# Kernel tuning notes

Measured on AMD Instinct MI355X. Metric: run time of the kernel, lower is better.

## Reference

```python
import jax, jax.numpy as jnp
import numpy as np

B, T, H = 1024, 1024, 64


def _lstm_cell(x, h, c, w_ih, w_hh, b_ih, b_hh):
    # gates: [B, 4H] in PyTorch order i, f, g, o
    g = x @ w_ih.T + h @ w_hh.T + b_ih + b_hh
    i, f, gg, o = jnp.split(g, 4, axis=-1)
    i = jax.nn.sigmoid(i)
    f = jax.nn.sigmoid(f)
    gg = jnp.tanh(gg)
    o = jax.nn.sigmoid(o)
    c_new = f * c + i * gg
    h_new = o * jnp.tanh(c_new)
    return h_new, c_new


def setup_inputs() -> dict:
    key = jax.random.key(0)
    ks = jax.random.split(key, 12)
    s = 1.0 / np.sqrt(H)  # torch default init scale
    r = lambda k, shape: jax.random.normal(k, shape, dtype=jnp.float32) * s
    return {
        "x": jax.random.normal(ks[0], (B, T), dtype=jnp.float32),
        "w_ih1": r(ks[1], (4 * H, 1)),
        "w_hh1": r(ks[2], (4 * H, H)),
        "b_ih1": r(ks[3], (4 * H,)),
        "b_hh1": r(ks[4], (4 * H,)),
        "w_ih2": r(ks[5], (4 * H, H)),
        "w_hh2": r(ks[6], (4 * H, H)),
        "b_ih2": r(ks[7], (4 * H,)),
        "b_hh2": r(ks[8], (4 * H,)),
        "w_lin": r(ks[9], (1, H)),
        "b_lin": r(ks[10], (1,)),
        "future_preds": 0,
    }


def reference(x, w_ih1, w_hh1, b_ih1, b_hh1, w_ih2, w_hh2, b_ih2, b_hh2,
              w_lin, b_lin, future_preds):
    bsz = x.shape[0]
    h1 = jnp.zeros((bsz, H), x.dtype)
    c1 = jnp.zeros((bsz, H), x.dtype)
    h2 = jnp.zeros((bsz, H), x.dtype)
    c2 = jnp.zeros((bsz, H), x.dtype)

    def step(carry, x_t):
        h1, c1, h2, c2 = carry
        h1, c1 = _lstm_cell(x_t, h1, c1, w_ih1, w_hh1, b_ih1, b_hh1)
        h2, c2 = _lstm_cell(h1, h2, c2, w_ih2, w_hh2, b_ih2, b_hh2)
        out = h2 @ w_lin.T + b_lin  # [B, 1]
        return (h1, c1, h2, c2), out

    xs = x.T[:, :, None]  # [T, B, 1]
    carry, outs = jax.lax.scan(step, (h1, c1, h2, c2), xs)
    outputs = outs[:, :, 0].T  # [B, T]

    if future_preds > 0:
        last = outs[-1]  # [B, 1]

        def fstep(carry, _):
            h1, c1, h2, c2, prev = carry
            h1, c1 = _lstm_cell(prev, h1, c1, w_ih1, w_hh1, b_ih1, b_hh1)
            h2, c2 = _lstm_cell(h1, h2, c2, w_ih2, w_hh2, b_ih2, b_hh2)
            out = h2 @ w_lin.T + b_lin
            return (h1, c1, h2, c2, out), out

        _, fouts = jax.lax.scan(fstep, (*carry, last), None, length=future_preds)
        outputs = jnp.concatenate([outputs, fouts[:, :, 0].T], axis=1)

    return outputs
```

## Files before the change

kernel.cpp:

```cpp
#include <hip/hip_runtime.h>
#include <hip/hip_bf16.h>


typedef _Float16 f16x8 __attribute__((ext_vector_type(8)));
typedef float    f32x4 __attribute__((ext_vector_type(4)));

namespace {
constexpr int Bb = 1024;
constexpr int Tt = 1024;
constexpr int NBat = 4;
constexpr int HSTR = 72;
constexpr int XSTR = 1025;

__device__ __forceinline__ int srow(int row) {
    return row ^ ((row >> 3) & 7);
}
__device__ __forceinline__ float sigm(float x) {
    float e = __builtin_amdgcn_exp2f(-1.4426950408889634f * x);
    return __builtin_amdgcn_rcpf(1.0f + e);
}
__device__ __forceinline__ float tanh_f(float x) {
    float e = __builtin_amdgcn_exp2f(-2.8853900817779268f * x);
    return __builtin_amdgcn_rcpf(1.0f + e) * 2.0f - 1.0f;
}
__device__ __forceinline__ bool detect_f32(const void* w) {
    const unsigned short* p = (const unsigned short*)w;
    int sane = 0;
    for (int i = 0; i < 64; ++i) {
        int e = (p[2 * i] >> 7) & 0xFF;
        if (e >= 107 && e <= 129) ++sane;
    }
    return sane < 32;
}
__device__ __forceinline__ float ld(const void* p, int i, bool f32) {
    return f32 ? ((const float*)p)[i]
               : __bfloat162float(((const __hip_bfloat16*)p)[i]);
}
__device__ __forceinline__ void st(void* p, int i, float v, bool f32) {
    if (f32) ((float*)p)[i] = v;
    else     ((__hip_bfloat16*)p)[i] = __float2bfloat16(v);
}
}

__global__ __launch_bounds__(512, 1) void lstm2_kernel(
    const void* __restrict__ x,
    const void* __restrict__ w_ih1,
    const void* __restrict__ w_hh1,
    const void* __restrict__ b_ih1,
    const void* __restrict__ b_hh1,
    const void* __restrict__ w_ih2,
    const void* __restrict__ w_hh2,
    const void* __restrict__ b_ih2,
    const void* __restrict__ b_hh2,
    const void* __restrict__ w_lin,
    const void* __restrict__ b_lin,
    void* __restrict__ out)
{
    const int tid  = threadIdx.x;
    const int lane = tid & 63;
    const int w    = tid >> 6;
    const int gw   = w & 3;
    const bool isP = w < 4;
    const int m    = lane & 15;
    const int quad = lane >> 4;
    const int bb   = blockIdx.x * NBat;

    const bool f32 = detect_f32(w_hh1);

    __shared__ float                  xs[NBat * XSTR];
    __shared__ __align__(16) _Float16 h1buf[2][16 * HSTR];
    __shared__ __align__(16) _Float16 h2buf[2][16 * HSTR];
    __shared__ __align__(16) float    scr1[4][64 * 4];
    __shared__ __align__(16) float    scr2[4][64 * 4];
    __shared__ float                  headl[2][16];
    __shared__ float                  outbuf[NBat * Tt];

    for (int i = tid; i < NBat * 1024; i += 512)
        xs[(i >> 10) * XSTR + (i & 1023)] = ld(x, (bb + (i >> 10)) * Tt + (i & 1023), f32);
    for (int i = tid; i < 16 * HSTR; i += 512) {
        h1buf[0][i] = (_Float16)0; h1buf[1][i] = (_Float16)0;
        h2buf[0][i] = (_Float16)0; h2buf[1][i] = (_Float16)0;
    }

    const int arow = lane & 15;
    const int g_ld = arow & 3;
    const int u_ld = arow >> 2;
    f16x8 wfA[4][2], wfB[4][2];
    {
        const void* MA = isP ? w_hh1 : w_ih2;
#pragma unroll
        for (int q = 0; q < 4; ++q) {
            const int row = 64 * g_ld + 16 * gw + 4 * q + u_ld;
#pragma unroll
            for (int s = 0; s < 2; ++s) {
                const int base = row * 64 + 32 * s + quad * 8;
                if (f32) {
                    const float* A = (const float*)MA;
                    const float* B = (const float*)w_hh2;
#pragma unroll
                    for (int j = 0; j < 8; ++j) {
                        wfA[q][s][j] = (_Float16)A[base + j];
                        wfB[q][s][j] = isP ? (_Float16)0.0f : (_Float16)B[base + j];
                    }
                } else {
                    const __hip_bfloat16* A = (const __hip_bfloat16*)MA;
                    const __hip_bfloat16* B = (const __hip_bfloat16*)w_hh2;
#pragma unroll
                    for (int j = 0; j < 8; ++j) {
                        wfA[q][s][j] = (_Float16)__bfloat162float(A[base + j]);
                        wfB[q][s][j] = isP ? (_Float16)0.0f
                                           : (_Float16)__bfloat162float(B[base + j]);
                    }
                }
            }
        }
    }
    f32x4 bv[4], wxv[4];
#pragma unroll
    for (int q = 0; q < 4; ++q)
#pragma unroll
        for (int r = 0; r < 4; ++r) {
            const int row = 64 * r + 16 * gw + 4 * q + quad;
            bv[q][r] = isP ? (ld(b_ih1, row, f32) + ld(b_hh1, row, f32))
                           : (ld(b_ih2, row, f32) + ld(b_hh2, row, f32));
            wxv[q][r] = isP ? ld(w_ih1, row, f32) : 0.0f;
        }
    const int cb = lane >> 4;
    const int uo = lane & 15;
    const int cidx = srow(lane) * 4;
    const float wl_u = ld(w_lin, 16 * gw + uo, f32);
    const float blin = ld(b_lin, 0, f32);
    float cst = 0.0f;
    __syncthreads();

    for (int t = 0; t <= Tt; ++t) {
        if (isP) {
            if (t < Tt) {
                f32x4 acc[4];
                const float xt = xs[(m & (NBat - 1)) * XSTR + t];
#pragma unroll
                for (int q = 0; q < 4; ++q)
#pragma unroll
                    for (int r = 0; r < 4; ++r)
                        acc[q][r] = fmaf(xt, wxv[q][r], bv[q][r]);
                if (t > 0) {
                    const _Float16* hp = h1buf[(t - 1) & 1] + m * HSTR;
                    const f16x8 ba = *(const f16x8*)(hp + quad * 8);
                    const f16x8 bb2 = *(const f16x8*)(hp + 32 + quad * 8);
#pragma unroll
                    for (int q = 0; q < 4; ++q) {
                        acc[q] = __builtin_amdgcn_mfma_f32_16x16x32_f16(wfA[q][0], ba, acc[q], 0, 0, 0);
                        acc[q] = __builtin_amdgcn_mfma_f32_16x16x32_f16(wfA[q][1], bb2, acc[q], 0, 0, 0);
                    }
                }
                if (m < NBat)
#pragma unroll
                    for (int q = 0; q < 4; ++q)
                        *(f32x4*)&scr1[gw][srow(m * 16 + q * 4 + quad) * 4] = acc[q];
                const f32x4 g = *(const f32x4*)&scr1[gw][cidx];
                float ig = sigm(g[0]), fg = sigm(g[1]);
                float gg = tanh_f(g[2]), og = sigm(g[3]);
                cst = fmaf(fg, cst, ig * gg);
                h1buf[t & 1][cb * HSTR + 16 * gw + uo] = (_Float16)(og * tanh_f(cst));
            }
        } else {
            if (t > 0) {
                if (t > 1 && w == 4 && lane < NBat) {
                    float s = blin;
#pragma unroll
                    for (int k = 0; k < 4; ++k) s += headl[t & 1][k * 4 + lane];
                    outbuf[lane * Tt + (t - 2)] = s;
                }
                const _Float16* h1p = h1buf[(t - 1) & 1] + m * HSTR;
                const _Float16* h2p = h2buf[t & 1] + m * HSTR;
                const f16x8 b1a = *(const f16x8*)(h1p + quad * 8);
                const f16x8 b1b = *(const f16x8*)(h1p + 32 + quad * 8);
                const f16x8 b2a = *(const f16x8*)(h2p + quad * 8);
                const f16x8 b2b = *(const f16x8*)(h2p + 32 + quad * 8);
                f32x4 acc[4];
#pragma unroll
                for (int q = 0; q < 4; ++q) {
                    f32x4 p2 = __builtin_amdgcn_mfma_f32_16x16x32_f16(wfA[q][0], b1a, bv[q], 0, 0, 0);
                    p2 = __builtin_amdgcn_mfma_f32_16x16x32_f16(wfA[q][1], b1b, p2, 0, 0, 0);
                    f32x4 p3 = __builtin_amdgcn_mfma_f32_16x16x32_f16(wfB[q][0], b2a, f32x4{0,0,0,0}, 0, 0, 0);
                    p3 = __builtin_amdgcn_mfma_f32_16x16x32_f16(wfB[q][1], b2b, p3, 0, 0, 0);
                    acc[q] = p2 + p3;
                }
                if (m < NBat)
#pragma unroll
                    for (int q = 0; q < 4; ++q)
                        *(f32x4*)&scr2[gw][srow(m * 16 + q * 4 + quad) * 4] = acc[q];
                const f32x4 g = *(const f32x4*)&scr2[gw][cidx];
                float ig = sigm(g[0]), fg = sigm(g[1]);
                float gg = tanh_f(g[2]), og = sigm(g[3]);
                cst = fmaf(fg, cst, ig * gg);
                float h = og * tanh_f(cst);
                h2buf[(t - 1) & 1][cb * HSTR + 16 * gw + uo] = (_Float16)h;
                float p = h * wl_u;
                p += __shfl_xor(p, 1); p += __shfl_xor(p, 2);
                p += __shfl_xor(p, 4); p += __shfl_xor(p, 8);
                if (uo == 0) headl[(t - 1) & 1][gw * 4 + cb] = p;
            }
        }
        __syncthreads();
    }

    if (w == 4 && lane < NBat) {
        float s = blin;
#pragma unroll
        for (int k = 0; k < 4; ++k) s += headl[(Tt - 1) & 1][k * 4 + lane];
        outbuf[lane * Tt + (Tt - 1)] = s;
    }
    __syncthreads();
    for (int i = tid; i < NBat * Tt; i += 512)
        st(out, (bb + (i >> 10)) * Tt + (i & 1023), outbuf[i], f32);
}

extern "C" void kernel_launch(void* const* d_in, const int* in_sizes, int n_in,
                              void* d_out, int out_size, void* d_ws, size_t ws_size,
                              hipStream_t stream)
{
    (void)in_sizes; (void)n_in; (void)out_size; (void)d_ws; (void)ws_size;
    lstm2_kernel<<<dim3(Bb / NBat), dim3(512), 0, stream>>>(
        d_in[0], d_in[1], d_in[2], d_in[3], d_in[4], d_in[5],
        d_in[6], d_in[7], d_in[8], d_in[9], d_in[10], d_out);
}
```

Before: 786.9 us.

## Prescale gate weights for exp2, use DPP reductions, setprio and guarded LDS loads

Folds the -log2(e) (or -2log2(e) for the cell gate) factors into the fp16 weights, biases and input weights, so each activation skips a multiply. The head reduction uses DPP row_shr steps instead of shuffle xor, with the result read from lane 15. Adds s_setprio around the MFMA blocks, precomputes the swizzled scratch addresses, limits the LDS B-operand loads to m<NBat, and unrolls the time loop by 2. Scaling the weights before the fp16 conversion slightly changes rounding, and the unroll raises register pressure.

```diff
diff --git a/kernel.cpp b/kernel.cpp
--- a/kernel.cpp
+++ b/kernel.cpp
@@ -15,13 +15,20 @@
 __device__ __forceinline__ int srow(int row) {
     return row ^ ((row >> 3) & 7);
 }
-__device__ __forceinline__ float sigm(float x) {
-    float e = __builtin_amdgcn_exp2f(-1.4426950408889634f * x);
-    return __builtin_amdgcn_rcpf(1.0f + e);
+__device__ __forceinline__ float sigm_pre(float a) {
+    return __builtin_amdgcn_rcpf(1.0f + __builtin_amdgcn_exp2f(a));
+}
+__device__ __forceinline__ float tanh_pre(float a) {
+    return fmaf(2.0f, __builtin_amdgcn_rcpf(1.0f + __builtin_amdgcn_exp2f(a)), -1.0f);
 }
 __device__ __forceinline__ float tanh_f(float x) {
     float e = __builtin_amdgcn_exp2f(-2.8853900817779268f * x);
-    return __builtin_amdgcn_rcpf(1.0f + e) * 2.0f - 1.0f;
+    return fmaf(2.0f, __builtin_amdgcn_rcpf(1.0f + e), -1.0f);
+}
+template <int CTRL>
+__device__ __forceinline__ float dpp_sum_step(float p) {
+    int v = __builtin_amdgcn_update_dpp(0, __float_as_int(p), CTRL, 0xf, 0xf, true);
+    return p + __int_as_float(v);
 }
 __device__ __forceinline__ bool detect_f32(const void* w) {
     const unsigned short* p = (const unsigned short*)w;
@@ -85,6 +92,7 @@
     const int arow = lane & 15;
     const int g_ld = arow & 3;
     const int u_ld = arow >> 2;
+    const float scA = (g_ld == 2) ? -2.8853900817779268f : -1.4426950408889634f;
     f16x8 wfA[4][2], wfB[4][2];
     {
         const void* MA = isP ? w_hh1 : w_ih2;
@@ -99,17 +107,18 @@
                     const float* B = (const float*)w_hh2;
 #pragma unroll
                     for (int j = 0; j < 8; ++j) {
-                        wfA[q][s][j] = (_Float16)A[base + j];
-                        wfB[q][s][j] = isP ? (_Float16)0.0f : (_Float16)B[base + j];
+                        wfA[q][s][j] = (_Float16)(scA * A[base + j]);
+                        wfB[q][s][j] = isP ? (_Float16)0.0f
+                                           : (_Float16)(scA * B[base + j]);
                     }
                 } else {
                     const __hip_bfloat16* A = (const __hip_bfloat16*)MA;
                     const __hip_bfloat16* B = (const __hip_bfloat16*)w_hh2;
 #pragma unroll
                     for (int j = 0; j < 8; ++j) {
-                        wfA[q][s][j] = (_Float16)__bfloat162float(A[base + j]);
+                        wfA[q][s][j] = (_Float16)(scA * __bfloat162float(A[base + j]));
                         wfB[q][s][j] = isP ? (_Float16)0.0f
-                                           : (_Float16)__bfloat162float(B[base + j]);
+                                           : (_Float16)(scA * __bfloat162float(B[base + j]));
                     }
                 }
             }
@@ -121,18 +130,24 @@
 #pragma unroll
         for (int r = 0; r < 4; ++r) {
             const int row = 64 * r + 16 * gw + 4 * q + quad;
-            bv[q][r] = isP ? (ld(b_ih1, row, f32) + ld(b_hh1, row, f32))
-                           : (ld(b_ih2, row, f32) + ld(b_hh2, row, f32));
-            wxv[q][r] = isP ? ld(w_ih1, row, f32) : 0.0f;
+            const float sg = (r == 2) ? -2.8853900817779268f : -1.4426950408889634f;
+            bv[q][r] = sg * (isP ? (ld(b_ih1, row, f32) + ld(b_hh1, row, f32))
+                                 : (ld(b_ih2, row, f32) + ld(b_hh2, row, f32)));
+            wxv[q][r] = isP ? sg * ld(w_ih1, row, f32) : 0.0f;
         }
     const int cb = lane >> 4;
     const int uo = lane & 15;
     const int cidx = srow(lane) * 4;
+    int swadr[4];
+#pragma unroll
+    for (int q = 0; q < 4; ++q) swadr[q] = srow(m * 16 + q * 4 + quad) * 4;
     const float wl_u = ld(w_lin, 16 * gw + uo, f32);
     const float blin = ld(b_lin, 0, f32);
     float cst = 0.0f;
+    f16x8 pa0{}, pa1{}, pb0{}, pb1{};
     __syncthreads();
 
+#pragma unroll 2
     for (int t = 0; t <= Tt; ++t) {
         if (isP) {
             if (t < Tt) {
@@ -145,21 +160,25 @@
                         acc[q][r] = fmaf(xt, wxv[q][r], bv[q][r]);
                 if (t > 0) {
                     const _Float16* hp = h1buf[(t - 1) & 1] + m * HSTR;
-                    const f16x8 ba = *(const f16x8*)(hp + quad * 8);
-                    const f16x8 bb2 = *(const f16x8*)(hp + 32 + quad * 8);
+                    if (m < NBat) {
+                        pa0 = *(const f16x8*)(hp + quad * 8);
+                        pa1 = *(const f16x8*)(hp + 32 + quad * 8);
+                    }
+                    __builtin_amdgcn_s_setprio(1);
 #pragma unroll
                     for (int q = 0; q < 4; ++q) {
-                        acc[q] = __builtin_amdgcn_mfma_f32_16x16x32_f16(wfA[q][0], ba, acc[q], 0, 0, 0);
-                        acc[q] = __builtin_amdgcn_mfma_f32_16x16x32_f16(wfA[q][1], bb2, acc[q], 0, 0, 0);
-                    }
+                        acc[q] = __builtin_amdgcn_mfma_f32_16x16x32_f16(wfA[q][0], pa0, acc[q], 0, 0, 0);
+                        acc[q] = __builtin_amdgcn_mfma_f32_16x16x32_f16(wfA[q][1], pa1, acc[q], 0, 0, 0);
+                    }
+                    __builtin_amdgcn_s_setprio(0);
                 }
                 if (m < NBat)
 #pragma unroll
                     for (int q = 0; q < 4; ++q)
-                        *(f32x4*)&scr1[gw][srow(m * 16 + q * 4 + quad) * 4] = acc[q];
+                        *(f32x4*)&scr1[gw][swadr[q]] = acc[q];
                 const f32x4 g = *(const f32x4*)&scr1[gw][cidx];
-                float ig = sigm(g[0]), fg = sigm(g[1]);
-                float gg = tanh_f(g[2]), og = sigm(g[3]);
+                float ig = sigm_pre(g[0]), fg = sigm_pre(g[1]);
+                float gg = tanh_pre(g[2]), og = sigm_pre(g[3]);
                 cst = fmaf(fg, cst, ig * gg);
                 h1buf[t & 1][cb * HSTR + 16 * gw + uo] = (_Float16)(og * tanh_f(cst));
             }
@@ -173,33 +192,39 @@
                 }
                 const _Float16* h1p = h1buf[(t - 1) & 1] + m * HSTR;
                 const _Float16* h2p = h2buf[t & 1] + m * HSTR;
-                const f16x8 b1a = *(const f16x8*)(h1p + quad * 8);
-                const f16x8 b1b = *(const f16x8*)(h1p + 32 + quad * 8);
-                const f16x8 b2a = *(const f16x8*)(h2p + quad * 8);
-                const f16x8 b2b = *(const f16x8*)(h2p + 32 + quad * 8);
+                if (m < NBat) {
+                    pa0 = *(const f16x8*)(h1p + quad * 8);
+                    pa1 = *(const f16x8*)(h1p + 32 + quad * 8);
+                    pb0 = *(const f16x8*)(h2p + quad * 8);
+                    pb1 = *(const f16x8*)(h2p + 32 + quad * 8);
+                }
                 f32x4 acc[4];
+                __builtin_amdgcn_s_setprio(1);
 #pragma unroll
                 for (int q = 0; q < 4; ++q) {
-                    f32x4 p2 = __builtin_amdgcn_mfma_f32_16x16x32_f16(wfA[q][0], b1a, bv[q], 0, 0, 0);
-                    p2 = __builtin_amdgcn_mfma_f32_16x16x32_f16(wfA[q][1], b1b, p2, 0, 0, 0);
-                    f32x4 p3 = __builtin_amdgcn_mfma_f32_16x16x32_f16(wfB[q][0], b2a, f32x4{0,0,0,0}, 0, 0, 0);
-                    p3 = __builtin_amdgcn_mfma_f32_16x16x32_f16(wfB[q][1], b2b, p3, 0, 0, 0);
+                    f32x4 p2 = __builtin_amdgcn_mfma_f32_16x16x32_f16(wfA[q][0], pa0, bv[q], 0, 0, 0);
+                    p2 = __builtin_amdgcn_mfma_f32_16x16x32_f16(wfA[q][1], pa1, p2, 0, 0, 0);
+                    f32x4 p3 = __builtin_amdgcn_mfma_f32_16x16x32_f16(wfB[q][0], pb0, f32x4{0,0,0,0}, 0, 0, 0);
+                    p3 = __builtin_amdgcn_mfma_f32_16x16x32_f16(wfB[q][1], pb1, p3, 0, 0, 0);
                     acc[q] = p2 + p3;
                 }
+                __builtin_amdgcn_s_setprio(0);
                 if (m < NBat)
 #pragma unroll
                     for (int q = 0; q < 4; ++q)
-                        *(f32x4*)&scr2[gw][srow(m * 16 + q * 4 + quad) * 4] = acc[q];
+                        *(f32x4*)&scr2[gw][swadr[q]] = acc[q];
                 const f32x4 g = *(const f32x4*)&scr2[gw][cidx];
-                float ig = sigm(g[0]), fg = sigm(g[1]);
-                float gg = tanh_f(g[2]), og = sigm(g[3]);
+                float ig = sigm_pre(g[0]), fg = sigm_pre(g[1]);
+                float gg = tanh_pre(g[2]), og = sigm_pre(g[3]);
                 cst = fmaf(fg, cst, ig * gg);
                 float h = og * tanh_f(cst);
                 h2buf[(t - 1) & 1][cb * HSTR + 16 * gw + uo] = (_Float16)h;
                 float p = h * wl_u;
-                p += __shfl_xor(p, 1); p += __shfl_xor(p, 2);
-                p += __shfl_xor(p, 4); p += __shfl_xor(p, 8);
-                if (uo == 0) headl[(t - 1) & 1][gw * 4 + cb] = p;
+                p = dpp_sum_step<0x111>(p);
+                p = dpp_sum_step<0x112>(p);
+                p = dpp_sum_step<0x114>(p);
+                p = dpp_sum_step<0x118>(p);
+                if (uo == 15) headl[(t - 1) & 1][gw * 4 + cb] = p;
             }
         }
         __syncthreads();
```

Measured after the change: 780.0 us. About the same (-0.9%).
